# Kernel optimization log

Hardware: AMD Instinct MI355X
Metric: run time of the kernel (lower is better)

Reference implementation:

```python
import jax, jax.numpy as jnp
import numpy as np

B, S = 32, 8192
HE, HD = 256, 256  # encoder_hidden_size, decoder_hidden_size


def setup_inputs() -> dict:
    key = jax.random.key(0)
    ks = jax.random.split(key, 8)
    scale = 1.0 / np.sqrt(HD)
    scale_e = 1.0 / np.sqrt(HE)
    return {
        "query": jax.random.normal(ks[0], (B, 1, HD), dtype=jnp.float32),
        "keys": jax.random.normal(ks[1], (B, S, HE), dtype=jnp.float32),
        "Wa_w": jax.random.uniform(ks[2], (HD, HD), jnp.float32, -scale, scale),
        "Wa_b": jax.random.uniform(ks[3], (HD,), jnp.float32, -scale, scale),
        "Ua_w": jax.random.uniform(ks[4], (HD, HE), jnp.float32, -scale_e, scale_e),
        "Ua_b": jax.random.uniform(ks[5], (HD,), jnp.float32, -scale_e, scale_e),
        "Va_w": jax.random.uniform(ks[6], (1, HD), jnp.float32, -scale, scale),
        "Va_b": jax.random.uniform(ks[7], (1,), jnp.float32, -scale, scale),
    }


def reference(query, keys, Wa_w, Wa_b, Ua_w, Ua_b, Va_w, Va_b):
    # q_proj: [B, 1, HD]; k_proj: [B, S, HD]
    q_proj = jnp.einsum("bqd,hd->bqh", query, Wa_w) + Wa_b
    k_proj = jnp.einsum("bse,he->bsh", keys, Ua_w) + Ua_b
    # scores: [B, S] -> [B, 1, S]
    scores = jnp.einsum("bsh,h->bs", jnp.tanh(q_proj + k_proj), Va_w[0]) + Va_b[0]
    weights = jax.nn.softmax(scores, axis=-1)[:, None, :]  # [B, 1, S]
    context = jnp.einsum("bqs,bse->bqe", weights, keys)    # [B, 1, HE]
    return (context, weights)
```

## Files before the change

kernel.cpp:

```cpp
#include <hip/hip_runtime.h>
#include <hip/hip_bf16.h>
#include <stdint.h>

#define B_ 32
#define S_ 8192
#define HD_ 256
#define HE_ 256
#define CHUNK 256
#define ROWS 16
#define MSTEPS (CHUNK/ROWS)
#define NCHUNK (S_/CHUNK)
#define TILE (ROWS * 512)

typedef __attribute__((ext_vector_type(8))) short bf16x8;
typedef __attribute__((ext_vector_type(4))) float f32x4;

__device__ __forceinline__ uint32_t cvt_pk_bf16(float lo, float hi) {
  uint32_t r;
  asm("v_cvt_pk_bf16_f32 %0, %1, %2" : "=v"(r) : "v"(lo), "v"(hi));
  return r;
}
__device__ __forceinline__ float bf2f(unsigned short h) {
  return __uint_as_float(((uint32_t)h) << 16);
}
__device__ __forceinline__ float tanh_fast(float x) {
  float e = __expf(2.0f * x);
  return 1.0f - 2.0f * __builtin_amdgcn_rcpf(e + 1.0f);
}
template<int CTRL>
__device__ __forceinline__ float dpp_shr_add(float v) {
  int t = __builtin_amdgcn_update_dpp(0, __float_as_int(v), CTRL, 0xf, 0xf, true);
  return v + __int_as_float(t);
}
__device__ __forceinline__ float row16_sum(float v) {
  v = dpp_shr_add<0x118>(v);
  v = dpp_shr_add<0x114>(v);
  v = dpp_shr_add<0x112>(v);
  v = dpp_shr_add<0x111>(v);
  return v;
}

__global__ void prep_kernel(const float* __restrict__ query,
                            const float* __restrict__ Wa_w,
                            const float* __restrict__ Wa_b,
                            const float* __restrict__ Ua_w,
                            const float* __restrict__ Ua_b,
                            float* __restrict__ qv,
                            unsigned short* __restrict__ ua_bf) {
  const int blk = blockIdx.x, t = threadIdx.x;
  if (blk < B_) {
    __shared__ float qs[HD_];
    qs[t] = query[blk * HD_ + t];
    __syncthreads();
    const float* wr = Wa_w + (size_t)t * HD_;
    float s = Wa_b[t] + Ua_b[t];
#pragma unroll 8
    for (int d = 0; d < HD_; ++d) s += qs[d] * wr[d];
    qv[blk * HD_ + t] = s;
  } else {
    const int base = (blk - B_) * 2048 + t * 8;
    float4 v0 = *(const float4*)(Ua_w + base);
    float4 v1 = *(const float4*)(Ua_w + base + 4);
    uint4 pk;
    pk.x = cvt_pk_bf16(v0.x, v0.y);
    pk.y = cvt_pk_bf16(v0.z, v0.w);
    pk.z = cvt_pk_bf16(v1.x, v1.y);
    pk.w = cvt_pk_bf16(v1.z, v1.w);
    *(uint4*)(ua_bf + base) = pk;
  }
}

__global__ __launch_bounds__(512)
__attribute__((amdgpu_waves_per_eu(4, 4)))
void main_kernel(const float* __restrict__ keys,
                 const float* __restrict__ qv,
                 const float* __restrict__ Va_w,
                 const unsigned short* __restrict__ ua_bf,
                 float* __restrict__ wexp_g,
                 float* __restrict__ partials) {
  __shared__ __align__(16) char kt[4 * TILE];
  __shared__ float sc3[3][16];
  __shared__ __align__(16) float num_l[8][64][4];

  const int t = threadIdx.x;
  const int b = blockIdx.y;
  const int chunk = blockIdx.x;
  const int s0 = chunk * CHUNK;
  const int lane = t & 63;
  const int w = t >> 6;
  const int ln = lane & 15;
  const int hi = lane >> 4;

  const unsigned short* ub0 = ua_bf + (size_t)(w * 32 + ln) * HE_ + hi * 8;
  const unsigned short* ub1 = ub0 + 16 * HE_;
  bf16x8 bb0[8], bb1[8];
#pragma unroll
  for (int k = 0; k < 8; ++k) {
    bb0[k] = *(const bf16x8*)(ub0 + k * 32);
    bb1[k] = *(const bf16x8*)(ub1 + k * 32);
  }
  const float q0  = qv[b * HD_ + w * 32 + ln];
  const float q1  = qv[b * HD_ + w * 32 + 16 + ln];
  const float va0 = Va_w[w * 32 + ln];
  const float va1 = Va_w[w * 32 + 16 + ln];

  const int srow = t >> 5;
  const int scch = t & 31;
  const float* ksrc = keys + ((size_t)b * S_ + s0 + srow) * HE_ + scch * 8;
  const int ldsoff = srow * 512 + ((scch * 16) ^ ((srow & 7) << 4));

  if (t < 48) ((float*)sc3)[t] = 0.f;
  {
    float4 a0 = *(const float4*)(ksrc);
    float4 a1 = *(const float4*)(ksrc + 4);
    uint4 pk;
    pk.x = cvt_pk_bf16(a0.x, a0.y);
    pk.y = cvt_pk_bf16(a0.z, a0.w);
    pk.z = cvt_pk_bf16(a1.x, a1.y);
    pk.w = cvt_pk_bf16(a1.z, a1.w);
    *(uint4*)(kt + ldsoff) = pk;
  }
  __syncthreads();

  const int asw = (ln & 7) << 4;
  const int nsw = (w & 7) << 4;
  float num4[4] = {0.f, 0.f, 0.f, 0.f};

  for (int i = 0; i < MSTEPS; ++i) {
    char* cur = kt + (i & 3) * TILE;
    char* stg = kt + ((i + 1) & 3) * TILE;
    char* prv = kt + ((i + 3) & 3) * TILE;

    float4 ga0, ga1;
    if (i + 1 < MSTEPS) {
      const float* kA = ksrc + (size_t)(i + 1) * ROWS * HE_;
      ga0 = *(const float4*)(kA);
      ga1 = *(const float4*)(kA + 4);
    }

    f32x4 a00 = {0.f,0.f,0.f,0.f}, a01 = {0.f,0.f,0.f,0.f};
    const char* arow = cur + ln * 512;
#pragma unroll
    for (int k = 0; k < 8; ++k) {
      bf16x8 af = *(const bf16x8*)(arow + ((k * 64 + hi * 16) ^ asw));
      a00 = __builtin_amdgcn_mfma_f32_16x16x32_bf16(af, bb0[k], a00, 0, 0, 0);
      a01 = __builtin_amdgcn_mfma_f32_16x16x32_bf16(af, bb1[k], a01, 0, 0, 0);
    }

    if (i > 0) {
      const float* scp = sc3[(i + 2) % 3];
      const float e0 = __expf(scp[w]);
      const float e8 = __expf(scp[w + 8]);
      if (lane == 0) {
        float* wg = wexp_g + (size_t)b * S_ + s0 + (i - 1) * ROWS;
        wg[w] = e0;
        wg[w + 8] = e8;
      }
      uint2 kv0 = *(const uint2*)(prv + w * 512 + ((lane * 8) ^ nsw));
      uint2 kv1 = *(const uint2*)(prv + (w + 8) * 512 + ((lane * 8) ^ nsw));
      num4[0] += e0 * bf2f((unsigned short)(kv0.x & 0xffff)) + e8 * bf2f((unsigned short)(kv1.x & 0xffff));
      num4[1] += e0 * bf2f((unsigned short)(kv0.x >> 16))    + e8 * bf2f((unsigned short)(kv1.x >> 16));
      num4[2] += e0 * bf2f((unsigned short)(kv0.y & 0xffff)) + e8 * bf2f((unsigned short)(kv1.y & 0xffff));
      num4[3] += e0 * bf2f((unsigned short)(kv0.y >> 16))    + e8 * bf2f((unsigned short)(kv1.y >> 16));
    }

#pragma unroll
    for (int r = 0; r < 4; ++r) {
      float v = tanh_fast(a00[r] + q0) * va0 + tanh_fast(a01[r] + q1) * va1;
      v = row16_sum(v);
      if (ln == 15) atomicAdd(&sc3[i % 3][hi * 4 + r], v);
    }

    if (t < 16) sc3[(i + 1) % 3][t] = 0.f;

    if (i + 1 < MSTEPS) {
      uint4 pk;
      pk.x = cvt_pk_bf16(ga0.x, ga0.y);
      pk.y = cvt_pk_bf16(ga0.z, ga0.w);
      pk.z = cvt_pk_bf16(ga1.x, ga1.y);
      pk.w = cvt_pk_bf16(ga1.z, ga1.w);
      *(uint4*)(stg + ldsoff) = pk;
    }
    __syncthreads();
  }

  {
    const float* scp = sc3[(MSTEPS - 1) % 3];
    const char* prv = kt + ((MSTEPS - 1) & 3) * TILE;
    const float e0 = __expf(scp[w]);
    const float e8 = __expf(scp[w + 8]);
    if (lane == 0) {
      float* wg = wexp_g + (size_t)b * S_ + s0 + (MSTEPS - 1) * ROWS;
      wg[w] = e0;
      wg[w + 8] = e8;
    }
    uint2 kv0 = *(const uint2*)(prv + w * 512 + ((lane * 8) ^ nsw));
    uint2 kv1 = *(const uint2*)(prv + (w + 8) * 512 + ((lane * 8) ^ nsw));
    num4[0] += e0 * bf2f((unsigned short)(kv0.x & 0xffff)) + e8 * bf2f((unsigned short)(kv1.x & 0xffff));
    num4[1] += e0 * bf2f((unsigned short)(kv0.x >> 16))    + e8 * bf2f((unsigned short)(kv1.x >> 16));
    num4[2] += e0 * bf2f((unsigned short)(kv0.y & 0xffff)) + e8 * bf2f((unsigned short)(kv1.y & 0xffff));
    num4[3] += e0 * bf2f((unsigned short)(kv0.y >> 16))    + e8 * bf2f((unsigned short)(kv1.y >> 16));
  }

  *(float4*)&num_l[w][lane][0] = make_float4(num4[0], num4[1], num4[2], num4[3]);
  __syncthreads();
  if (t < 256) {
    float s = 0.f;
#pragma unroll
    for (int ww = 0; ww < 8; ++ww) s += num_l[ww][t >> 2][t & 3];
    partials[((size_t)b * NCHUNK + chunk) * 256 + t] = s;
  }
}

__global__ void combine_kernel(const float* __restrict__ wexp_g,
                               const float* __restrict__ partials,
                               float* __restrict__ out) {
  __shared__ float red[4];
  __shared__ float rdsh;
  const int b = blockIdx.x, t = threadIdx.x;
  const float* we = wexp_g + (size_t)b * S_;
  float s = 0.f;
#pragma unroll 4
  for (int i = t; i < S_; i += 256) s += we[i];
#pragma unroll
  for (int mm = 32; mm; mm >>= 1) s += __shfl_xor(s, mm, 64);
  if ((t & 63) == 0) red[t >> 6] = s;
  __syncthreads();
  if (t == 0) rdsh = 1.0f / (red[0] + red[1] + red[2] + red[3]);
  __syncthreads();
  const float rd = rdsh;

  const float* pb = partials + (size_t)b * NCHUNK * 256;
  float num = 0.f;
#pragma unroll 4
  for (int i = 0; i < NCHUNK; ++i) num += pb[i * 256 + t];
  out[b * HE_ + t] = num * rd;

  float* wout = out + B_ * HE_ + (size_t)b * S_;
#pragma unroll 4
  for (int i = t; i < S_; i += 256) wout[i] = we[i] * rd;
}

extern "C" void kernel_launch(void* const* d_in, const int* in_sizes, int n_in,
                              void* d_out, int out_size, void* d_ws, size_t ws_size,
                              hipStream_t stream) {
  const float* query = (const float*)d_in[0];
  const float* keys  = (const float*)d_in[1];
  const float* Wa_w  = (const float*)d_in[2];
  const float* Wa_b  = (const float*)d_in[3];
  const float* Ua_w  = (const float*)d_in[4];
  const float* Ua_b  = (const float*)d_in[5];
  const float* Va_w  = (const float*)d_in[6];
  float* out = (float*)d_out;

  char* ws = (char*)d_ws;
  float* qv             = (float*)ws;
  unsigned short* ua_bf = (unsigned short*)(ws + 32 * 1024);
  float* wexp_g         = (float*)(ws + 160 * 1024);
  float* partials       = (float*)(ws + 160 * 1024 + 1048576);

  prep_kernel<<<64, 256, 0, stream>>>(query, Wa_w, Wa_b, Ua_w, Ua_b, qv, ua_bf);
  dim3 g(NCHUNK, B_);
  main_kernel<<<g, 512, 0, stream>>>(keys, qv, Va_w, ua_bf, wexp_g, partials);
  combine_kernel<<<B_, 256, 0, stream>>>(wexp_g, partials, out);
}
```

Before: 81.05 us.

## Stage fp32 keys via direct global-to-LDS loads with two-deep async prefetch

Keys are now copied straight from global memory into LDS as fp32 through global_load_lds, with a swizzled layout, instead of going through registers and being packed to bf16 before the store. Prefetch is two tiles ahead, and the per-step barriers become explicit vmcnt waits. The bf16 conversion moves to the MFMA operand fetch, and the context accumulation reads fp32 from LDS, so the context sum also gains precision. Per-row exp weights are buffered in LDS and written to global memory once per block. The cost is a doubled LDS footprint (4×16KB) and extra conversion work inside the inner loop.

```diff
diff --git a/kernel.cpp b/kernel.cpp
--- a/kernel.cpp
+++ b/kernel.cpp
@@ -10,7 +10,7 @@
 #define ROWS 16
 #define MSTEPS (CHUNK/ROWS)
 #define NCHUNK (S_/CHUNK)
-#define TILE (ROWS * 512)
+#define TILEB (ROWS * 1024)
 
 typedef __attribute__((ext_vector_type(8))) short bf16x8;
 typedef __attribute__((ext_vector_type(4))) float f32x4;
@@ -19,9 +19,6 @@
   uint32_t r;
   asm("v_cvt_pk_bf16_f32 %0, %1, %2" : "=v"(r) : "v"(lo), "v"(hi));
   return r;
-}
-__device__ __forceinline__ float bf2f(unsigned short h) {
-  return __uint_as_float(((uint32_t)h) << 16);
 }
 __device__ __forceinline__ float tanh_fast(float x) {
   float e = __expf(2.0f * x);
@@ -39,6 +36,15 @@
   v = dpp_shr_add<0x111>(v);
   return v;
 }
+__device__ __forceinline__ void gload16(const float* g, char* lds) {
+  __builtin_amdgcn_global_load_lds(
+      (const __attribute__((address_space(1))) void*)g,
+      (__attribute__((address_space(3))) void*)lds, 16, 0, 0);
+}
+#define WAITBAR(VM) do { \
+  asm volatile("s_waitcnt vmcnt(" #VM ") lgkmcnt(0)\n\ts_barrier" ::: "memory"); \
+  __builtin_amdgcn_sched_barrier(0); \
+} while (0)
 
 __global__ void prep_kernel(const float* __restrict__ query,
                             const float* __restrict__ Wa_w,
@@ -78,8 +84,9 @@
                  const unsigned short* __restrict__ ua_bf,
                  float* __restrict__ wexp_g,
                  float* __restrict__ partials) {
-  __shared__ __align__(16) char kt[4 * TILE];
+  __shared__ __align__(16) char kt[4 * TILEB];
   __shared__ float sc3[3][16];
+  __shared__ float wexp_l[CHUNK];
   __shared__ __align__(16) float num_l[8][64][4];
 
   const int t = threadIdx.x;
@@ -104,47 +111,49 @@
   const float va0 = Va_w[w * 32 + ln];
   const float va1 = Va_w[w * 32 + 16 + ln];
 
-  const int srow = t >> 5;
-  const int scch = t & 31;
-  const float* ksrc = keys + ((size_t)b * S_ + s0 + srow) * HE_ + scch * 8;
-  const int ldsoff = srow * 512 + ((scch * 16) ^ ((srow & 7) << 4));
+  const int r0 = 2 * w, r1 = 2 * w + 1;
+  const float* gsrc0 = keys + ((size_t)b * S_ + s0 + r0) * HE_ + (((lane * 16) ^ ((r0 & 7) << 4)) >> 2);
+  const float* gsrc1 = keys + ((size_t)b * S_ + s0 + r1) * HE_ + (((lane * 16) ^ ((r1 & 7) << 4)) >> 2);
+  char* ldst0 = kt + r0 * 1024;
+  char* ldst1 = kt + r1 * 1024;
 
   if (t < 48) ((float*)sc3)[t] = 0.f;
-  {
-    float4 a0 = *(const float4*)(ksrc);
-    float4 a1 = *(const float4*)(ksrc + 4);
-    uint4 pk;
-    pk.x = cvt_pk_bf16(a0.x, a0.y);
-    pk.y = cvt_pk_bf16(a0.z, a0.w);
-    pk.z = cvt_pk_bf16(a1.x, a1.y);
-    pk.w = cvt_pk_bf16(a1.z, a1.w);
-    *(uint4*)(kt + ldsoff) = pk;
-  }
-  __syncthreads();
-
-  const int asw = (ln & 7) << 4;
+  gload16(gsrc0, ldst0);
+  gload16(gsrc1, ldst1);
+  gload16(gsrc0 + ROWS * HE_, ldst0 + TILEB);
+  gload16(gsrc1 + ROWS * HE_, ldst1 + TILEB);
+  WAITBAR(2);
+
+  const int s_ln = (ln & 7) << 4;
   const int nsw = (w & 7) << 4;
   float num4[4] = {0.f, 0.f, 0.f, 0.f};
 
+#pragma unroll
   for (int i = 0; i < MSTEPS; ++i) {
-    char* cur = kt + (i & 3) * TILE;
-    char* stg = kt + ((i + 1) & 3) * TILE;
-    char* prv = kt + ((i + 3) & 3) * TILE;
-
-    float4 ga0, ga1;
-    if (i + 1 < MSTEPS) {
-      const float* kA = ksrc + (size_t)(i + 1) * ROWS * HE_;
-      ga0 = *(const float4*)(kA);
-      ga1 = *(const float4*)(kA + 4);
+    char* cur = kt + (i & 3) * TILEB;
+    char* prv = kt + ((i + 3) & 3) * TILEB;
+
+    if (i + 2 < MSTEPS) {
+      const size_t adv = (size_t)(i + 2) * ROWS * HE_;
+      char* dst = kt + ((i + 2) & 3) * TILEB;
+      gload16(gsrc0 + adv, dst + r0 * 1024);
+      gload16(gsrc1 + adv, dst + r1 * 1024);
     }
 
     f32x4 a00 = {0.f,0.f,0.f,0.f}, a01 = {0.f,0.f,0.f,0.f};
-    const char* arow = cur + ln * 512;
+    const char* arow = cur + ln * 1024;
 #pragma unroll
     for (int k = 0; k < 8; ++k) {
-      bf16x8 af = *(const bf16x8*)(arow + ((k * 64 + hi * 16) ^ asw));
-      a00 = __builtin_amdgcn_mfma_f32_16x16x32_bf16(af, bb0[k], a00, 0, 0, 0);
-      a01 = __builtin_amdgcn_mfma_f32_16x16x32_bf16(af, bb1[k], a01, 0, 0, 0);
+      const int bse = k * 128 + hi * 32;
+      float4 fA = *(const float4*)(arow + (bse ^ s_ln));
+      float4 fB = *(const float4*)(arow + ((bse + 16) ^ s_ln));
+      union { bf16x8 v; uint32_t u[4]; } af;
+      af.u[0] = cvt_pk_bf16(fA.x, fA.y);
+      af.u[1] = cvt_pk_bf16(fA.z, fA.w);
+      af.u[2] = cvt_pk_bf16(fB.x, fB.y);
+      af.u[3] = cvt_pk_bf16(fB.z, fB.w);
+      a00 = __builtin_amdgcn_mfma_f32_16x16x32_bf16(af.v, bb0[k], a00, 0, 0, 0);
+      a01 = __builtin_amdgcn_mfma_f32_16x16x32_bf16(af.v, bb1[k], a01, 0, 0, 0);
     }
 
     if (i > 0) {
@@ -152,16 +161,15 @@
       const float e0 = __expf(scp[w]);
       const float e8 = __expf(scp[w + 8]);
       if (lane == 0) {
-        float* wg = wexp_g + (size_t)b * S_ + s0 + (i - 1) * ROWS;
-        wg[w] = e0;
-        wg[w + 8] = e8;
+        wexp_l[(i - 1) * ROWS + w] = e0;
+        wexp_l[(i - 1) * ROWS + 8 + w] = e8;
       }
-      uint2 kv0 = *(const uint2*)(prv + w * 512 + ((lane * 8) ^ nsw));
-      uint2 kv1 = *(const uint2*)(prv + (w + 8) * 512 + ((lane * 8) ^ nsw));
-      num4[0] += e0 * bf2f((unsigned short)(kv0.x & 0xffff)) + e8 * bf2f((unsigned short)(kv1.x & 0xffff));
-      num4[1] += e0 * bf2f((unsigned short)(kv0.x >> 16))    + e8 * bf2f((unsigned short)(kv1.x >> 16));
-      num4[2] += e0 * bf2f((unsigned short)(kv0.y & 0xffff)) + e8 * bf2f((unsigned short)(kv1.y & 0xffff));
-      num4[3] += e0 * bf2f((unsigned short)(kv0.y >> 16))    + e8 * bf2f((unsigned short)(kv1.y >> 16));
+      const float4 kv0 = *(const float4*)(prv + w * 1024 + ((lane * 16) ^ nsw));
+      const float4 kv1 = *(const float4*)(prv + (w + 8) * 1024 + ((lane * 16) ^ nsw));
+      num4[0] += e0 * kv0.x + e8 * kv1.x;
+      num4[1] += e0 * kv0.y + e8 * kv1.y;
+      num4[2] += e0 * kv0.z + e8 * kv1.z;
+      num4[3] += e0 * kv0.w + e8 * kv1.w;
     }
 
 #pragma unroll
@@ -173,38 +181,30 @@
 
     if (t < 16) sc3[(i + 1) % 3][t] = 0.f;
 
-    if (i + 1 < MSTEPS) {
-      uint4 pk;
-      pk.x = cvt_pk_bf16(ga0.x, ga0.y);
-      pk.y = cvt_pk_bf16(ga0.z, ga0.w);
-      pk.z = cvt_pk_bf16(ga1.x, ga1.y);
-      pk.w = cvt_pk_bf16(ga1.z, ga1.w);
-      *(uint4*)(stg + ldsoff) = pk;
-    }
-    __syncthreads();
+    if (i < MSTEPS - 2) WAITBAR(2); else WAITBAR(0);
   }
 
   {
     const float* scp = sc3[(MSTEPS - 1) % 3];
-    const char* prv = kt + ((MSTEPS - 1) & 3) * TILE;
+    const char* prv = kt + ((MSTEPS - 1) & 3) * TILEB;
     const float e0 = __expf(scp[w]);
     const float e8 = __expf(scp[w + 8]);
     if (lane == 0) {
-      float* wg = wexp_g + (size_t)b * S_ + s0 + (MSTEPS - 1) * ROWS;
-      wg[w] = e0;
-      wg[w + 8] = e8;
-    }
-    uint2 kv0 = *(const uint2*)(prv + w * 512 + ((lane * 8) ^ nsw));
-    uint2 kv1 = *(const uint2*)(prv + (w + 8) * 512 + ((lane * 8) ^ nsw));
-    num4[0] += e0 * bf2f((unsigned short)(kv0.x & 0xffff)) + e8 * bf2f((unsigned short)(kv1.x & 0xffff));
-    num4[1] += e0 * bf2f((unsigned short)(kv0.x >> 16))    + e8 * bf2f((unsigned short)(kv1.x >> 16));
-    num4[2] += e0 * bf2f((unsigned short)(kv0.y & 0xffff)) + e8 * bf2f((unsigned short)(kv1.y & 0xffff));
-    num4[3] += e0 * bf2f((unsigned short)(kv0.y >> 16))    + e8 * bf2f((unsigned short)(kv1.y >> 16));
+      wexp_l[(MSTEPS - 1) * ROWS + w] = e0;
+      wexp_l[(MSTEPS - 1) * ROWS + 8 + w] = e8;
+    }
+    const float4 kv0 = *(const float4*)(prv + w * 1024 + ((lane * 16) ^ nsw));
+    const float4 kv1 = *(const float4*)(prv + (w + 8) * 1024 + ((lane * 16) ^ nsw));
+    num4[0] += e0 * kv0.x + e8 * kv1.x;
+    num4[1] += e0 * kv0.y + e8 * kv1.y;
+    num4[2] += e0 * kv0.z + e8 * kv1.z;
+    num4[3] += e0 * kv0.w + e8 * kv1.w;
   }
 
   *(float4*)&num_l[w][lane][0] = make_float4(num4[0], num4[1], num4[2], num4[3]);
   __syncthreads();
   if (t < 256) {
+    wexp_g[(size_t)b * S_ + s0 + t] = wexp_l[t];
     float s = 0.f;
 #pragma unroll
     for (int ww = 0; ww < 8; ++ww) s += num_l[ww][t >> 2][t & 3];
```

After: 200.0 us. 147% more time.
